# Kernel tuning notes

Hardware: AMD Instinct MI355X
Metric: run time of the kernel (lower is better)

The kernel has to match this reference:

```python
import jax, jax.numpy as jnp
import numpy as np

B, R, H = 64, 32, 1024  # batch, num_rounds, lstm_hidden_size
IN = 2 * H              # GatedTrans in_dim
EPS = 1e-12             # F.normalize eps


def _gated(x, Wy, by, Wg, bg):
    # GatedTrans: tanh branch * leaky_relu branch (slope 0.01, torch default)
    return jnp.tanh(x @ Wy + by) * jax.nn.leaky_relu(x @ Wg + bg, 0.01)


def setup_inputs() -> dict:
    key = jax.random.key(0)
    ks = jax.random.split(key, 12)
    s_in = 1.0 / np.sqrt(IN)
    s_h = 1.0 / np.sqrt(H)
    return {
        "hist": jax.random.normal(ks[0], (B, R, IN), jnp.float32),
        "ques": jax.random.normal(ks[1], (B, R, IN), jnp.float32),
        "W_hy": jax.random.normal(ks[2], (IN, H), jnp.float32) * s_in,
        "b_hy": jnp.zeros((H,), jnp.float32),
        "W_hg": jax.random.normal(ks[3], (IN, H), jnp.float32) * s_in,
        "b_hg": jnp.zeros((H,), jnp.float32),
        "W_qy": jax.random.normal(ks[4], (IN, H), jnp.float32) * s_in,
        "b_qy": jnp.zeros((H,), jnp.float32),
        "W_qg": jax.random.normal(ks[5], (IN, H), jnp.float32) * s_in,
        "b_qg": jnp.zeros((H,), jnp.float32),
        "W_att": jax.random.normal(ks[6], (H,), jnp.float32) * s_h,
        "b_att": jnp.zeros((), jnp.float32),
    }


def reference(hist, ques, W_hy, b_hy, W_hg, b_hg, W_qy, b_qy, W_qg, b_qg, W_att, b_att):
    hist_embed = _gated(hist, W_hy, b_hy, W_hg, b_hg)   # [B, R, H]
    ques_embed = _gated(ques, W_qy, b_qy, W_qg, b_qg)   # [B, R, H]
    # broadcast outer product over rounds: [B, Rq, Rh, H]
    att_embed = ques_embed[:, :, None, :] * hist_embed[:, None, :, :]
    norm = jnp.sqrt(jnp.sum(att_embed * att_embed, axis=-1, keepdims=True))
    att_embed = att_embed / jnp.maximum(norm, EPS)       # F.normalize(p=2)
    scores = att_embed @ W_att + b_att                   # [B, Rq, Rh]
    att = jax.nn.softmax(scores, axis=-1)
    tril = jnp.tril(jnp.ones((R, R), jnp.float32))       # causal round mask
    att_masked = att * tril
    att_masked = att_masked / jnp.sum(att_masked, axis=-1, keepdims=True)
    # weighted sum over hist rounds: [B, Rq, 2H]
    feat = jnp.einsum("bqh,bhd->bqd", att_masked, hist)
    return feat
```

## Files before the change

kernel.cpp:

```cpp
#include <hip/hip_runtime.h>
#include <cstdint>

#define IN_DIM 2048
#define H_DIM  1024
#define BROWS  2048
#define BATCH  64
#define ROUNDS 32

typedef __bf16 bf16x8 __attribute__((ext_vector_type(8)));
typedef float  f32x4  __attribute__((ext_vector_type(4)));
typedef unsigned short u16;
typedef u16 u16x8 __attribute__((ext_vector_type(8)));

__device__ __forceinline__ u16 f2bf(float f) {
    unsigned int u = __float_as_uint(f);
    u += 0x7FFFu + ((u >> 16) & 1u);
    return (u16)(u >> 16);
}

__device__ __forceinline__ void async_ld16(const void* g, void* l) {
    __builtin_amdgcn_global_load_lds(
        (__attribute__((address_space(1))) void*)(uintptr_t)g,
        (__attribute__((address_space(3))) void*)(unsigned int)(uintptr_t)l,
        16, 0, 0);
}

#define BAR()    asm volatile("s_barrier" ::: "memory")
#define LGKM0()  asm volatile("s_waitcnt lgkmcnt(0)" ::: "memory")
#define VMCNT6() asm volatile("s_waitcnt vmcnt(6)" ::: "memory")
#define VMCNT0() asm volatile("s_waitcnt vmcnt(0)" ::: "memory")

__global__ __launch_bounds__(256) void prep(
    const float* __restrict__ hist, const float* __restrict__ ques,
    u16* __restrict__ xh, u16* __restrict__ xq,
    const float* __restrict__ why, const float* __restrict__ whg,
    const float* __restrict__ wqy, const float* __restrict__ wqg,
    u16* __restrict__ oh, u16* __restrict__ oq)
{
    int idx = blockIdx.x;
    if (idx < 4096) {
        int i = idx * 256 + threadIdx.x;
        const float4* h4 = (const float4*)hist;
        const float4* q4 = (const float4*)ques;
        float4 a = h4[i], b = q4[i];
        ushort4 oa, ob;
        oa.x = f2bf(a.x); oa.y = f2bf(a.y); oa.z = f2bf(a.z); oa.w = f2bf(a.w);
        ob.x = f2bf(b.x); ob.y = f2bf(b.y); ob.z = f2bf(b.z); ob.w = f2bf(b.w);
        ((ushort4*)xh)[i] = oa;
        ((ushort4*)xq)[i] = ob;
        return;
    }
    int zz = idx - 4096;
    int z  = zz >> 9;
    int rem = zz & 511;
    int bk = rem >> 5;
    int bn = rem & 31;
    const float* Y = z == 0 ? why : wqy;
    const float* G = z == 0 ? whg : wqg;
    u16* O = z == 0 ? oh : oq;
    int k0 = bk << 7, c0 = bn << 5, n0 = bn << 6;

    __shared__ float t[2][128][33];
    int tid = threadIdx.x;
    int row = tid >> 3, cg = (tid & 7) << 2;
    #pragma unroll
    for (int p = 0; p < 4; p++) {
        int k = row + 32 * p;
        float4 vy = *(const float4*)&Y[(size_t)(k0 + k) * H_DIM + c0 + cg];
        float4 vg = *(const float4*)&G[(size_t)(k0 + k) * H_DIM + c0 + cg];
        t[0][k][cg + 0] = vy.x; t[0][k][cg + 1] = vy.y;
        t[0][k][cg + 2] = vy.z; t[0][k][cg + 3] = vy.w;
        t[1][k][cg + 0] = vg.x; t[1][k][cg + 1] = vg.y;
        t[1][k][cg + 2] = vg.z; t[1][k][cg + 3] = vg.w;
    }
    __syncthreads();
    int j4 = tid >> 4, kg = tid & 15;
    #pragma unroll
    for (int p = 0; p < 4; p++) {
        int j = j4 + 16 * p;
        int mat = (j >> 4) & 1;
        int lc = ((j >> 5) << 4) | (j & 15);
        u16x8 pk;
        #pragma unroll
        for (int e = 0; e < 8; e++)
            pk[e] = f2bf(t[mat][kg * 8 + e][lc]);
        *(u16x8*)&O[(size_t)(n0 + j) * IN_DIM + k0 + kg * 8] = pk;
    }
}

__global__ __launch_bounds__(512, 2) void gemm_act(
    const u16* __restrict__ xh, const u16* __restrict__ xq,
    const u16* __restrict__ wth, const u16* __restrict__ wtq,
    const float* __restrict__ bhy, const float* __restrict__ bhg,
    const float* __restrict__ bqy, const float* __restrict__ bqg,
    u16* __restrict__ eh, u16* __restrict__ eq)
{
    int L = blockIdx.x;
    int cluster = L & 7;
    int slot = L >> 3;
    int z = cluster >> 2;
    int y = (cluster & 1) * 4 + (slot >> 3);
    int x = ((cluster >> 1) & 1) * 8 + (slot & 7);
    int m0 = y * 256, n0 = x * 128;

    const u16* A  = z == 0 ? xh : xq;
    const u16* Bt = z == 0 ? wth : wtq;
    const float* by = z == 0 ? bhy : bqy;
    const float* bg = z == 0 ? bhg : bqg;
    u16* E = z == 0 ? eh : eq;

    __shared__ __align__(16) u16 As[2][256 * 64];
    __shared__ __align__(16) u16 Bs[2][128 * 64];

    int tid = threadIdx.x;
    int wave = tid >> 6, lane = tid & 63;
    int lane15 = lane & 15, quad = lane >> 4;
    int wm = (wave & 3) * 64;
    int wn = (wave >> 2) * 64;

    f32x4 acc[4][4];
    #pragma unroll
    for (int i = 0; i < 4; i++)
        #pragma unroll
        for (int j = 0; j < 4; j++) acc[i][j] = (f32x4){0.f, 0.f, 0.f, 0.f};

    int sArow[4], sAkc[4], sAcb[4];
    #pragma unroll
    for (int r2 = 0; r2 < 4; r2++) {
        int cbase = r2 * 512 + wave * 64;
        int cs = cbase + lane;
        int row = cs >> 3, s = cs & 7;
        sArow[r2] = row; sAkc[r2] = s ^ (row & 7); sAcb[r2] = cbase;
    }
    int sBrow[2], sBkc[2], sBcb[2];
    #pragma unroll
    for (int r2 = 0; r2 < 2; r2++) {
        int cbase = r2 * 512 + wave * 64;
        int cs = cbase + lane;
        int row = cs >> 3, s = cs & 7;
        sBrow[r2] = row; sBkc[r2] = s ^ (row & 7); sBcb[r2] = cbase;
    }

    #define STAGE(buf, kt)                                                                    \
        _Pragma("unroll")                                                                     \
        for (int r2 = 0; r2 < 4; r2++)                                                        \
            async_ld16(A + (size_t)(m0 + sArow[r2]) * IN_DIM + (kt) + sAkc[r2] * 8,           \
                       &As[buf][sAcb[r2] * 8]);                                               \
        _Pragma("unroll")                                                                     \
        for (int r2 = 0; r2 < 2; r2++)                                                        \
            async_ld16(Bt + (size_t)(n0 + sBrow[r2]) * IN_DIM + (kt) + sBkc[r2] * 8,          \
                       &Bs[buf][sBcb[r2] * 8]);

    bf16x8 a0[4], b0[4], a1[4], b1[4];

    #define DSREAD(da, db, buf, ks)                                                           \
        _Pragma("unroll")                                                                     \
        for (int i = 0; i < 4; i++) {                                                         \
            int row = wm + i * 16 + lane15;                                                   \
            int s = ((ks) * 4 + quad) ^ (row & 7);                                            \
            da[i] = *(const bf16x8*)&As[buf][row * 64 + s * 8];                               \
            int rowb = wn + i * 16 + lane15;                                                  \
            int sb = ((ks) * 4 + quad) ^ (rowb & 7);                                          \
            db[i] = *(const bf16x8*)&Bs[buf][rowb * 64 + sb * 8];                             \
        }

    #define MFMA16(fa, fb)                                                                    \
        __builtin_amdgcn_s_setprio(1);                                                        \
        _Pragma("unroll")                                                                     \
        for (int i = 0; i < 4; i++)                                                           \
            _Pragma("unroll")                                                                 \
            for (int j = 0; j < 4; j++)                                                       \
                acc[i][j] = __builtin_amdgcn_mfma_f32_16x16x32_bf16(                          \
                    fa[i], fb[j], acc[i][j], 0, 0, 0);                                        \
        __builtin_amdgcn_s_setprio(0);

    STAGE(0, 0)
    STAGE(1, 64)
    VMCNT6(); BAR();
    DSREAD(a0, b0, 0, 0)

    #pragma unroll 1
    for (int kt = 0; kt < IN_DIM; kt += 128) {
        DSREAD(a1, b1, 0, 1)
        MFMA16(a0, b0)
        LGKM0(); BAR();
        if (kt + 128 < IN_DIM) { STAGE(0, kt + 128) VMCNT6(); }
        else                   { VMCNT0(); }
        BAR();
        DSREAD(a0, b0, 1, 0)
        MFMA16(a1, b1)
        DSREAD(a1, b1, 1, 1)
        MFMA16(a0, b0)
        if (kt + 128 < IN_DIM) {
            LGKM0(); BAR();
            STAGE(1, kt + 192)
            VMCNT6(); BAR();
            DSREAD(a0, b0, 0, 0)
        }
        MFMA16(a1, b1)
    }
    #undef STAGE
    #undef DSREAD
    #undef MFMA16

    int n0w = n0 + wn;
    #pragma unroll
    for (int jp = 0; jp < 2; jp++) {
        int hc = (n0w >> 1) + jp * 16 + lane15;
        float vy = by[hc], vg = bg[hc];
        #pragma unroll
        for (int i = 0; i < 4; i++) {
            #pragma unroll
            for (int r = 0; r < 4; r++) {
                int row = m0 + wm + i * 16 + quad * 4 + r;
                float y2 = tanhf(acc[i][2 * jp][r] + vy);
                float g = acc[i][2 * jp + 1][r] + vg;
                E[(size_t)row * H_DIM + hc] = f2bf(y2 * (g > 0.f ? g : 0.01f * g));
            }
        }
    }
}

__global__ __launch_bounds__(256) void score_feat(
    const u16* __restrict__ eh, const u16* __restrict__ eq,
    const float* __restrict__ hist, const float* __restrict__ watt,
    const float* __restrict__ batt, float* __restrict__ out)
{
    int idx = blockIdx.x;
    int b = idx & 63, q = idx >> 6;
    int tid = threadIdx.x, wave = tid >> 6, lane = tid & 63;
    __shared__ float sw[32], swn[32];

    const u16* qe = eq + (size_t)(b * ROUNDS + q) * H_DIM;
    float uw[16], u2[16];
    #pragma unroll
    for (int c = 0; c < 2; c++) {
        uint4 pk = ((const uint4*)qe)[lane + 64 * c];
        float4 w0 = ((const float4*)watt)[(lane + 64 * c) * 2];
        float4 w1 = ((const float4*)watt)[(lane + 64 * c) * 2 + 1];
        unsigned int ws[4] = {pk.x, pk.y, pk.z, pk.w};
        float wf[8] = {w0.x, w0.y, w0.z, w0.w, w1.x, w1.y, w1.z, w1.w};
        #pragma unroll
        for (int e = 0; e < 4; e++) {
            float lo = __uint_as_float(ws[e] << 16);
            float hi = __uint_as_float(ws[e] & 0xFFFF0000u);
            uw[c * 8 + 2 * e]     = lo * wf[2 * e];
            u2[c * 8 + 2 * e]     = lo * lo;
            uw[c * 8 + 2 * e + 1] = hi * wf[2 * e + 1];
            u2[c * 8 + 2 * e + 1] = hi * hi;
        }
    }
    for (int h = wave; h <= q; h += 4) {
        const u16* he = eh + (size_t)(b * ROUNDS + h) * H_DIM;
        float num = 0.f, nrm = 0.f;
        #pragma unroll
        for (int c = 0; c < 2; c++) {
            uint4 pk = ((const uint4*)he)[lane + 64 * c];
            unsigned int vs[4] = {pk.x, pk.y, pk.z, pk.w};
            #pragma unroll
            for (int e = 0; e < 4; e++) {
                float lo = __uint_as_float(vs[e] << 16);
                float hi = __uint_as_float(vs[e] & 0xFFFF0000u);
                num += uw[c * 8 + 2 * e] * lo + uw[c * 8 + 2 * e + 1] * hi;
                nrm += u2[c * 8 + 2 * e] * lo * lo + u2[c * 8 + 2 * e + 1] * hi * hi;
            }
        }
        #pragma unroll
        for (int off = 32; off > 0; off >>= 1) {
            num += __shfl_down(num, off);
            nrm += __shfl_down(nrm, off);
        }
        if (lane == 0)
            sw[h] = num / fmaxf(sqrtf(nrm), 1e-12f) + batt[0];
    }
    __syncthreads();
    if (tid < 64) {
        int h = lane & 31;
        bool v = (h <= q);
        float s = v ? sw[h] : -1e30f;
        float mx = s;
        #pragma unroll
        for (int off = 16; off > 0; off >>= 1)
            mx = fmaxf(mx, __shfl_xor(mx, off));
        float e = v ? expf(s - mx) : 0.f;
        float zs = e;
        #pragma unroll
        for (int off = 16; off > 0; off >>= 1)
            zs += __shfl_xor(zs, off);
        if (v && lane < 32) swn[h] = e / zs;
    }
    __syncthreads();
    const float4* hb = (const float4*)(hist + (size_t)b * ROUNDS * IN_DIM);
    float4* ob = (float4*)(out + (size_t)(b * ROUNDS + q) * IN_DIM);
    #pragma unroll
    for (int d0 = 0; d0 < 2; d0++) {
        int d = tid + d0 * 256;
        float4 a = {0.f, 0.f, 0.f, 0.f};
        for (int h = 0; h <= q; h++) {
            float w = swn[h];
            float4 x = hb[h * 512 + d];
            a.x += w * x.x; a.y += w * x.y; a.z += w * x.z; a.w += w * x.w;
        }
        ob[d] = a;
    }
}

extern "C" void kernel_launch(void* const* d_in, const int* in_sizes, int n_in,
                              void* d_out, int out_size, void* d_ws, size_t ws_size,
                              hipStream_t stream) {
    const float* hist = (const float*)d_in[0];
    const float* ques = (const float*)d_in[1];
    const float* Why  = (const float*)d_in[2];
    const float* bhy  = (const float*)d_in[3];
    const float* Whg  = (const float*)d_in[4];
    const float* bhg  = (const float*)d_in[5];
    const float* Wqy  = (const float*)d_in[6];
    const float* bqy  = (const float*)d_in[7];
    const float* Wqg  = (const float*)d_in[8];
    const float* bqg  = (const float*)d_in[9];
    const float* watt = (const float*)d_in[10];
    const float* batt = (const float*)d_in[11];
    float* out = (float*)d_out;

    char* w = (char*)d_ws;
    u16* Xh  = (u16*)w;
    u16* Xq  = Xh  + (size_t)BROWS * IN_DIM;
    u16* WtH = Xq  + (size_t)BROWS * IN_DIM;
    u16* WtQ = WtH + (size_t)IN_DIM * IN_DIM;
    u16* Eh  = WtQ + (size_t)IN_DIM * IN_DIM;
    u16* Eq  = Eh  + (size_t)BROWS * H_DIM;

    prep<<<5120, 256, 0, stream>>>(hist, ques, Xh, Xq, Why, Whg, Wqy, Wqg, WtH, WtQ);
    gemm_act<<<256, 512, 0, stream>>>(Xh, Xq, WtH, WtQ, bhy, bhg, bqy, bqg, Eh, Eq);
    score_feat<<<2048, 256, 0, stream>>>(Eh, Eq, hist, watt, batt, out);
}
```

Measured before the change: 180.8 us.

## Shrink GEMM tiles to 128x128x32 with 256-thread blocks and double buffering

Reworks the gated GEMM from 256x128 tiles with K-step 64 and 512 threads to 128x128 tiles with K-step 32 and 256 threads. The grid doubles to 512 blocks and the LDS swizzle and staging pattern are redone for 32-wide rows. The aim is more blocks per CU and better load balance across the CUs. In exchange, each block reuses less data, needs more barriers per unit of K, and issues more global loads per FLOP.

```diff
diff --git a/kernel.cpp b/kernel.cpp
--- a/kernel.cpp
+++ b/kernel.cpp
@@ -27,7 +27,7 @@
 
 #define BAR()    asm volatile("s_barrier" ::: "memory")
 #define LGKM0()  asm volatile("s_waitcnt lgkmcnt(0)" ::: "memory")
-#define VMCNT6() asm volatile("s_waitcnt vmcnt(6)" ::: "memory")
+#define VMCNT4() asm volatile("s_waitcnt vmcnt(4)" ::: "memory")
 #define VMCNT0() asm volatile("s_waitcnt vmcnt(0)" ::: "memory")
 
 __global__ __launch_bounds__(256) void prep(
@@ -88,7 +88,7 @@
     }
 }
 
-__global__ __launch_bounds__(512, 2) void gemm_act(
+__global__ __launch_bounds__(256, 4) void gemm_act(
     const u16* __restrict__ xh, const u16* __restrict__ xq,
     const u16* __restrict__ wth, const u16* __restrict__ wtq,
     const float* __restrict__ bhy, const float* __restrict__ bhg,
@@ -99,9 +99,9 @@
     int cluster = L & 7;
     int slot = L >> 3;
     int z = cluster >> 2;
-    int y = (cluster & 1) * 4 + (slot >> 3);
+    int y = (cluster & 1) * 8 + (slot >> 3);
     int x = ((cluster >> 1) & 1) * 8 + (slot & 7);
-    int m0 = y * 256, n0 = x * 128;
+    int m0 = y * 128, n0 = x * 128;
 
     const u16* A  = z == 0 ? xh : xq;
     const u16* Bt = z == 0 ? wth : wtq;
@@ -109,14 +109,13 @@
     const float* bg = z == 0 ? bhg : bqg;
     u16* E = z == 0 ? eh : eq;
 
-    __shared__ __align__(16) u16 As[2][256 * 64];
-    __shared__ __align__(16) u16 Bs[2][128 * 64];
+    __shared__ __align__(16) u16 As[2][128 * 32];
+    __shared__ __align__(16) u16 Bs[2][128 * 32];
 
     int tid = threadIdx.x;
     int wave = tid >> 6, lane = tid & 63;
     int lane15 = lane & 15, quad = lane >> 4;
-    int wm = (wave & 3) * 64;
-    int wn = (wave >> 2) * 64;
+    int wm = (wave >> 1) * 64, wn = (wave & 1) * 64;
 
     f32x4 acc[4][4];
     #pragma unroll
@@ -124,84 +123,68 @@
         #pragma unroll
         for (int j = 0; j < 4; j++) acc[i][j] = (f32x4){0.f, 0.f, 0.f, 0.f};
 
-    int sArow[4], sAkc[4], sAcb[4];
-    #pragma unroll
-    for (int r2 = 0; r2 < 4; r2++) {
-        int cbase = r2 * 512 + wave * 64;
-        int cs = cbase + lane;
-        int row = cs >> 3, s = cs & 7;
-        sArow[r2] = row; sAkc[r2] = s ^ (row & 7); sAcb[r2] = cbase;
-    }
-    int sBrow[2], sBkc[2], sBcb[2];
+    int aoff[2], boff[2], cb[2];
     #pragma unroll
     for (int r2 = 0; r2 < 2; r2++) {
-        int cbase = r2 * 512 + wave * 64;
-        int cs = cbase + lane;
-        int row = cs >> 3, s = cs & 7;
-        sBrow[r2] = row; sBkc[r2] = s ^ (row & 7); sBcb[r2] = cbase;
+        int cs = r2 * 256 + tid;
+        int row = cs >> 2, p = cs & 3;
+        int l = p ^ ((row >> 1) & 3);
+        aoff[r2] = (m0 + row) * IN_DIM + l * 8;
+        boff[r2] = (n0 + row) * IN_DIM + l * 8;
+        cb[r2]   = r2 * 256 + wave * 64;
     }
 
     #define STAGE(buf, kt)                                                                    \
         _Pragma("unroll")                                                                     \
-        for (int r2 = 0; r2 < 4; r2++)                                                        \
-            async_ld16(A + (size_t)(m0 + sArow[r2]) * IN_DIM + (kt) + sAkc[r2] * 8,           \
-                       &As[buf][sAcb[r2] * 8]);                                               \
-        _Pragma("unroll")                                                                     \
-        for (int r2 = 0; r2 < 2; r2++)                                                        \
-            async_ld16(Bt + (size_t)(n0 + sBrow[r2]) * IN_DIM + (kt) + sBkc[r2] * 8,          \
-                       &Bs[buf][sBcb[r2] * 8]);
-
-    bf16x8 a0[4], b0[4], a1[4], b1[4];
-
-    #define DSREAD(da, db, buf, ks)                                                           \
+        for (int r2 = 0; r2 < 2; r2++) {                                                      \
+            async_ld16(A  + (size_t)aoff[r2] + (kt), &As[buf][cb[r2] * 8]);                   \
+            async_ld16(Bt + (size_t)boff[r2] + (kt), &Bs[buf][cb[r2] * 8]);                   \
+        }
+
+    bf16x8 af[4], bfv[4];
+
+    #define DSREAD(buf)                                                                       \
         _Pragma("unroll")                                                                     \
         for (int i = 0; i < 4; i++) {                                                         \
             int row = wm + i * 16 + lane15;                                                   \
-            int s = ((ks) * 4 + quad) ^ (row & 7);                                            \
-            da[i] = *(const bf16x8*)&As[buf][row * 64 + s * 8];                               \
+            int p = quad ^ ((row >> 1) & 3);                                                  \
+            af[i] = *(const bf16x8*)&As[buf][row * 32 + p * 8];                               \
             int rowb = wn + i * 16 + lane15;                                                  \
-            int sb = ((ks) * 4 + quad) ^ (rowb & 7);                                          \
-            db[i] = *(const bf16x8*)&Bs[buf][rowb * 64 + sb * 8];                             \
-        }
-
-    #define MFMA16(fa, fb)                                                                    \
+            int pb = quad ^ ((rowb >> 1) & 3);                                                \
+            bfv[i] = *(const bf16x8*)&Bs[buf][rowb * 32 + pb * 8];                            \
+        }
+
+    #define MFMA16()                                                                          \
         __builtin_amdgcn_s_setprio(1);                                                        \
         _Pragma("unroll")                                                                     \
         for (int i = 0; i < 4; i++)                                                           \
             _Pragma("unroll")                                                                 \
             for (int j = 0; j < 4; j++)                                                       \
                 acc[i][j] = __builtin_amdgcn_mfma_f32_16x16x32_bf16(                          \
-                    fa[i], fb[j], acc[i][j], 0, 0, 0);                                        \
+                    af[i], bfv[j], acc[i][j], 0, 0, 0);                                       \
         __builtin_amdgcn_s_setprio(0);
 
+    #define TILE(t, buf)                                                                      \
+        DSREAD(buf)                                                                           \
+        LGKM0(); BAR();                                                                       \
+        if ((t) + 2 < 64) { STAGE(buf, ((t) + 2) * 32) }                                      \
+        MFMA16()                                                                              \
+        if ((t) + 2 < 64) { VMCNT4(); } else { VMCNT0(); }                                    \
+        if ((t) < 63) { BAR(); }
+
     STAGE(0, 0)
-    STAGE(1, 64)
-    VMCNT6(); BAR();
-    DSREAD(a0, b0, 0, 0)
+    STAGE(1, 32)
+    VMCNT4(); BAR();
 
     #pragma unroll 1
-    for (int kt = 0; kt < IN_DIM; kt += 128) {
-        DSREAD(a1, b1, 0, 1)
-        MFMA16(a0, b0)
-        LGKM0(); BAR();
-        if (kt + 128 < IN_DIM) { STAGE(0, kt + 128) VMCNT6(); }
-        else                   { VMCNT0(); }
-        BAR();
-        DSREAD(a0, b0, 1, 0)
-        MFMA16(a1, b1)
-        DSREAD(a1, b1, 1, 1)
-        MFMA16(a0, b0)
-        if (kt + 128 < IN_DIM) {
-            LGKM0(); BAR();
-            STAGE(1, kt + 192)
-            VMCNT6(); BAR();
-            DSREAD(a0, b0, 0, 0)
-        }
-        MFMA16(a1, b1)
+    for (int t2 = 0; t2 < 64; t2 += 2) {
+        TILE(t2, 0)
+        TILE(t2 + 1, 1)
     }
     #undef STAGE
     #undef DSREAD
     #undef MFMA16
+    #undef TILE
 
     int n0w = n0 + wn;
     #pragma unroll
@@ -331,6 +314,6 @@
     u16* Eq  = Eh  + (size_t)BROWS * H_DIM;
 
     prep<<<5120, 256, 0, stream>>>(hist, ques, Xh, Xq, Why, Whg, Wqy, Wqg, WtH, WtQ);
-    gemm_act<<<256, 512, 0, stream>>>(Xh, Xq, WtH, WtQ, bhy, bhg, bqy, bqg, Eh, Eq);
+    gemm_act<<<512, 256, 0, stream>>>(Xh, Xq, WtH, WtQ, bhy, bhg, bqy, bqg, Eh, Eq);
     score_feat<<<2048, 256, 0, stream>>>(Eh, Eq, hist, watt, batt, out);
 }
```

Result: slower. 184.9 us (+2.3%).

## Process eight query rounds per block to reuse hist loads in score_feat

Applied to the files above, without the earlier changes.

score_feat now handles eight consecutive query rounds per block instead of one, cutting the grid from 2048 to 256 blocks. The weighted hist sum keeps eight accumulators per thread, so each hist row is loaded once per group instead of once per query. Softmax weights are stored transposed in shared memory so each h can read all eight weights with vector loads. In exchange, scoring is serialized per wave over whole h ranges, there are fewer blocks to spread across CUs, and register pressure rises.

```diff
diff --git a/kernel.cpp b/kernel.cpp
--- a/kernel.cpp
+++ b/kernel.cpp
@@ -227,57 +227,66 @@
     const float* __restrict__ batt, float* __restrict__ out)
 {
     int idx = blockIdx.x;
-    int b = idx & 63, q = idx >> 6;
+    int b = idx & 63, qg = idx >> 6;
+    int q0 = qg * 8, maxq = q0 + 7;
     int tid = threadIdx.x, wave = tid >> 6, lane = tid & 63;
-    __shared__ float sw[32], swn[32];
-
-    const u16* qe = eq + (size_t)(b * ROUNDS + q) * H_DIM;
-    float uw[16], u2[16];
-    #pragma unroll
-    for (int c = 0; c < 2; c++) {
-        uint4 pk = ((const uint4*)qe)[lane + 64 * c];
-        float4 w0 = ((const float4*)watt)[(lane + 64 * c) * 2];
-        float4 w1 = ((const float4*)watt)[(lane + 64 * c) * 2 + 1];
-        unsigned int ws[4] = {pk.x, pk.y, pk.z, pk.w};
-        float wf[8] = {w0.x, w0.y, w0.z, w0.w, w1.x, w1.y, w1.z, w1.w};
-        #pragma unroll
-        for (int e = 0; e < 4; e++) {
-            float lo = __uint_as_float(ws[e] << 16);
-            float hi = __uint_as_float(ws[e] & 0xFFFF0000u);
-            uw[c * 8 + 2 * e]     = lo * wf[2 * e];
-            u2[c * 8 + 2 * e]     = lo * lo;
-            uw[c * 8 + 2 * e + 1] = hi * wf[2 * e + 1];
-            u2[c * 8 + 2 * e + 1] = hi * hi;
-        }
-    }
-    for (int h = wave; h <= q; h += 4) {
-        const u16* he = eh + (size_t)(b * ROUNDS + h) * H_DIM;
-        float num = 0.f, nrm = 0.f;
+    __shared__ float sw[8][32];
+    __shared__ float wt[32][8];
+
+    ((float*)wt)[tid] = 0.f;
+
+    for (int qi = wave; qi < 8; qi += 4) {
+        int q = q0 + qi;
+        const u16* qe = eq + (size_t)(b * ROUNDS + q) * H_DIM;
+        float uw[16], u2[16];
         #pragma unroll
         for (int c = 0; c < 2; c++) {
-            uint4 pk = ((const uint4*)he)[lane + 64 * c];
-            unsigned int vs[4] = {pk.x, pk.y, pk.z, pk.w};
+            uint4 pk = ((const uint4*)qe)[lane + 64 * c];
+            float4 w0 = ((const float4*)watt)[(lane + 64 * c) * 2];
+            float4 w1 = ((const float4*)watt)[(lane + 64 * c) * 2 + 1];
+            unsigned int ws[4] = {pk.x, pk.y, pk.z, pk.w};
+            float wf[8] = {w0.x, w0.y, w0.z, w0.w, w1.x, w1.y, w1.z, w1.w};
             #pragma unroll
             for (int e = 0; e < 4; e++) {
-                float lo = __uint_as_float(vs[e] << 16);
-                float hi = __uint_as_float(vs[e] & 0xFFFF0000u);
-                num += uw[c * 8 + 2 * e] * lo + uw[c * 8 + 2 * e + 1] * hi;
-                nrm += u2[c * 8 + 2 * e] * lo * lo + u2[c * 8 + 2 * e + 1] * hi * hi;
-            }
-        }
-        #pragma unroll
-        for (int off = 32; off > 0; off >>= 1) {
-            num += __shfl_down(num, off);
-            nrm += __shfl_down(nrm, off);
-        }
-        if (lane == 0)
-            sw[h] = num / fmaxf(sqrtf(nrm), 1e-12f) + batt[0];
+                float lo = __uint_as_float(ws[e] << 16);
+                float hi = __uint_as_float(ws[e] & 0xFFFF0000u);
+                uw[c * 8 + 2 * e]     = lo * wf[2 * e];
+                u2[c * 8 + 2 * e]     = lo * lo;
+                uw[c * 8 + 2 * e + 1] = hi * wf[2 * e + 1];
+                u2[c * 8 + 2 * e + 1] = hi * hi;
+            }
+        }
+        for (int h = 0; h <= q; h++) {
+            const u16* he = eh + (size_t)(b * ROUNDS + h) * H_DIM;
+            float num = 0.f, nrm = 0.f;
+            #pragma unroll
+            for (int c = 0; c < 2; c++) {
+                uint4 pk = ((const uint4*)he)[lane + 64 * c];
+                unsigned int vs[4] = {pk.x, pk.y, pk.z, pk.w};
+                #pragma unroll
+                for (int e = 0; e < 4; e++) {
+                    float lo = __uint_as_float(vs[e] << 16);
+                    float hi = __uint_as_float(vs[e] & 0xFFFF0000u);
+                    num += uw[c * 8 + 2 * e] * lo + uw[c * 8 + 2 * e + 1] * hi;
+                    nrm += u2[c * 8 + 2 * e] * lo * lo + u2[c * 8 + 2 * e + 1] * hi * hi;
+                }
+            }
+            #pragma unroll
+            for (int off = 32; off > 0; off >>= 1) {
+                num += __shfl_down(num, off);
+                nrm += __shfl_down(nrm, off);
+            }
+            if (lane == 0)
+                sw[qi][h] = num / fmaxf(sqrtf(nrm), 1e-12f) + batt[0];
+        }
     }
     __syncthreads();
-    if (tid < 64) {
+
+    for (int qi = wave; qi < 8; qi += 4) {
+        int q = q0 + qi;
         int h = lane & 31;
         bool v = (h <= q);
-        float s = v ? sw[h] : -1e30f;
+        float s = v ? sw[qi][h] : -1e30f;
         float mx = s;
         #pragma unroll
         for (int off = 16; off > 0; off >>= 1)
@@ -287,21 +296,32 @@
         #pragma unroll
         for (int off = 16; off > 0; off >>= 1)
             zs += __shfl_xor(zs, off);
-        if (v && lane < 32) swn[h] = e / zs;
+        if (v && lane < 32) wt[h][qi] = e / zs;
     }
     __syncthreads();
+
     const float4* hb = (const float4*)(hist + (size_t)b * ROUNDS * IN_DIM);
-    float4* ob = (float4*)(out + (size_t)(b * ROUNDS + q) * IN_DIM);
-    #pragma unroll
-    for (int d0 = 0; d0 < 2; d0++) {
-        int d = tid + d0 * 256;
-        float4 a = {0.f, 0.f, 0.f, 0.f};
-        for (int h = 0; h <= q; h++) {
-            float w = swn[h];
-            float4 x = hb[h * 512 + d];
-            a.x += w * x.x; a.y += w * x.y; a.z += w * x.z; a.w += w * x.w;
-        }
-        ob[d] = a;
+    float4* ob = (float4*)(out + (size_t)(b * ROUNDS + q0) * IN_DIM);
+    #pragma unroll
+    for (int cc = 0; cc < 2; cc++) {
+        int c = tid + cc * 256;
+        float4 a[8];
+        #pragma unroll
+        for (int qi = 0; qi < 8; qi++) a[qi] = (float4){0.f, 0.f, 0.f, 0.f};
+        for (int h = 0; h <= maxq; h++) {
+            float4 x = hb[h * 512 + c];
+            float4 wa = *(const float4*)&wt[h][0];
+            float4 wb = *(const float4*)&wt[h][4];
+            float w8[8] = {wa.x, wa.y, wa.z, wa.w, wb.x, wb.y, wb.z, wb.w};
+            #pragma unroll
+            for (int qi = 0; qi < 8; qi++) {
+                a[qi].x += w8[qi] * x.x; a[qi].y += w8[qi] * x.y;
+                a[qi].z += w8[qi] * x.z; a[qi].w += w8[qi] * x.w;
+            }
+        }
+        #pragma unroll
+        for (int qi = 0; qi < 8; qi++)
+            ob[qi * 512 + c] = a[qi];
     }
 }
 
@@ -332,5 +352,5 @@
 
     prep<<<5120, 256, 0, stream>>>(hist, ques, Xh, Xq, Why, Whg, Wqy, Wqg, WtH, WtQ);
     gemm_act<<<256, 512, 0, stream>>>(Xh, Xq, WtH, WtQ, bhy, bhg, bqy, bqg, Eh, Eq);
-    score_feat<<<2048, 256, 0, stream>>>(Eh, Eq, hist, watt, batt, out);
-}
+    score_feat<<<256, 256, 0, stream>>>(Eh, Eq, hist, watt, batt, out);
+}
```

Result: slower. 210.4 us (+16.4%).
